# Optimization experiments

Measured on AMD Instinct MI355X. Metric: run time of the kernel, lower is better.

Reference implementation:

```python
import jax, jax.numpy as jnp
import numpy as np

GAMMA = 0.99
NUM_CODEWORDS = 512
CODEBOOK_DIM = 64


def setup_inputs() -> dict:
    key = jax.random.key(0)
    kx, kc = jax.random.split(key)
    x = jax.random.normal(kx, (32, 64, 64, 64), dtype=jnp.float32)  # [N,C,H,W]
    codebook = jax.random.normal(kc, (NUM_CODEWORDS, CODEBOOK_DIM), dtype=jnp.float32) / 2
    N_state = jnp.ones((NUM_CODEWORDS,), dtype=jnp.float32)
    m_state = codebook.copy()
    return {"x": x, "codebook": codebook, "N_state": N_state, "m_state": m_state}


def reference(x, codebook, N_state, m_state):
    N, C, H, W = x.shape
    K = codebook.shape[0]
    # flatten to tokens: [N*H*W, C]
    xf = jnp.transpose(x, (0, 2, 3, 1)).reshape(-1, C)
    d2 = (jnp.sum(xf * xf, axis=-1, keepdims=True)
          - 2.0 * (xf @ codebook.T)
          + jnp.sum(codebook * codebook, axis=-1)[None, :])
    index = jnp.argmin(d2, axis=1)  # [T]
    q = codebook[index].reshape(N, H, W, C).transpose(0, 3, 1, 2)  # [N,C,H,W]
    # straight-through estimator
    out = x + jax.lax.stop_gradient(q - x)
    # EMA update (training path, no_grad in original)
    counts = jax.ops.segment_sum(jnp.ones_like(index, dtype=x.dtype), index, num_segments=K)
    sums = jax.ops.segment_sum(xf, index, num_segments=K)  # [K,C]
    occupied = counts > 0
    N_new = jnp.where(occupied, N_state * GAMMA + counts * (1.0 - GAMMA), N_state)
    m_new = jnp.where(occupied[:, None], m_state * GAMMA + sums * (1.0 - GAMMA), m_state)
    codebook_new = m_new / N_new[:, None]
    return out, codebook_new, N_new, m_new
```

## Files before the change

kernel.cpp:

```cpp
#include <hip/hip_runtime.h>

static constexpr int Nn_ = 32, Cc_ = 64, Hh_ = 64, Ww_ = 64;
static constexpr int K_ = 512;
static constexpr int HW_ = Hh_ * Ww_;
static constexpr int CHW_ = Cc_ * HW_;
static constexpr int T_ = Nn_ * Hh_ * Ww_;
static constexpr int OUT_ELEMS = Nn_ * Cc_ * Hh_ * Ww_;
static constexpr int OFF_CB = OUT_ELEMS;
static constexpr int OFF_N  = OUT_ELEMS + 32768;
static constexpr int OFF_M  = OUT_ELEMS + 32768 + 512;

static constexpr int WS_IDX     = 0;
static constexpr int WS_FIXCNT  = T_;
static constexpr int WS_FIXLIST = T_ + 1;
static constexpr int WS_CBH     = 262148;
static constexpr int WS_CBL     = WS_CBH + 16384;
static constexpr int WS_CN      = WS_CBL + 16384;
static constexpr int WS_CNA     = WS_CN + 512;
static constexpr int WS_PART    = 295940;
static constexpr int SLICE_F    = K_ * Cc_ + K_;

static constexpr float THETA = 0.002f;

typedef _Float16 half8  __attribute__((ext_vector_type(8)));
typedef float    f32x16 __attribute__((ext_vector_type(16)));

__global__ __launch_bounds__(256) void k_prep(const float* __restrict__ cb,
                                              float* __restrict__ ws) {
    int j = blockIdx.x * 256 + threadIdx.x;
    if (j == 0) ((int*)(ws + WS_FIXCNT))[0] = 0;
    float v = cb[j];
    _Float16 h = (_Float16)v;
    _Float16 lo = (_Float16)(v - (float)h);
    ((_Float16*)(ws + WS_CBH))[j] = h;
    ((_Float16*)(ws + WS_CBL))[j] = lo;
    float sq = v * v;
#pragma unroll
    for (int m = 1; m < 64; m <<= 1) sq += __shfl_xor(sq, m);
    if ((threadIdx.x & 63) == 0) {
        int k = j >> 6;
        ws[WS_CN + k] = sq;
        int t = k >> 5, r5 = k & 31;
        int hi = (r5 >> 2) & 1;
        int reg = (r5 & 3) + 4 * (r5 >> 3);
        ws[WS_CNA + hi * 256 + t * 16 + reg] = sq;
    }
}

__global__ __launch_bounds__(256, 3) void k_assign(const float* __restrict__ x,
                                                   const float* __restrict__ cb,
                                                   float* __restrict__ ws,
                                                   float* __restrict__ out) {
    __shared__ alignas(16) unsigned char smem[52224];
    int* bi_s   = (int*)(smem + 51200);
    int* cert_s = (int*)(smem + 51712);

    const int b    = blockIdx.x;
    const int tid  = threadIdx.x;
    const int lane = tid & 63;
    const int wv   = tid >> 6;
    const int row0 = 2 * b, row1 = 2 * b + 1;
    const int xb0 = (row0 >> 6) * CHW_ + (row0 & 63) * Ww_;
    const int xb1 = (row1 >> 6) * CHW_ + (row1 & 63) * Ww_;

    {
        const int s  = tid & 31;
        const int c8 = tid >> 5;
        const int r  = s >> 4, wq = s & 15;
        half8 hp[4], lp[4];
#pragma unroll
        for (int stp = 0; stp < 8; ++stp) {
            int ch = c8 * 8 + stp;
            float4 v = *(const float4*)(x + (r ? xb1 : xb0) + ch * HW_ + 4 * wq);
            float vv[4] = {v.x, v.y, v.z, v.w};
#pragma unroll
            for (int j = 0; j < 4; ++j) {
                _Float16 h = (_Float16)vv[j];
                _Float16 lo = (_Float16)(vv[j] - (float)h);
                hp[j][stp] = h; lp[j][stp] = lo;
            }
        }
        const int blk = c8 ^ (wq & 7);
#pragma unroll
        for (int j = 0; j < 4; ++j) {
            int tt = 64 * r + 4 * wq + j;
            *(half8*)(smem + tt * 128 + blk * 16) = hp[j];
            *(half8*)(smem + 16384 + tt * 128 + blk * 16) = lp[j];
        }
        ((float*)(smem + 49152))[tid]       = ws[WS_CNA + tid];
        ((float*)(smem + 49152))[tid + 256] = ws[WS_CNA + tid + 256];
    }

    const char* cbh_g = (const char*)(ws + WS_CBH);
    const char* cbl_g = (const char*)(ws + WS_CBL);
    {
        float4 h4 = *(const float4*)(cbh_g + tid * 16);
        float4 l4 = *(const float4*)(cbl_g + tid * 16);
        int r = tid >> 3, p = (tid & 7) ^ (r & 7);
        *(float4*)(smem + 32768 + r * 128 + p * 16) = h4;
        *(float4*)(smem + 32768 + 4096 + r * 128 + p * 16) = l4;
    }
    __syncthreads();

    const int tb = 32 * wv + (lane & 31);
    const int hi = lane >> 5;
    half8 bh[4], bl[4];
    {
        const int tsw = (tb >> 2) & 7;
#pragma unroll
        for (int ks = 0; ks < 4; ++ks) {
            int blk = (2 * ks + hi) ^ tsw;
            bh[ks] = *(const half8*)(smem + tb * 128 + blk * 16);
            bl[ks] = *(const half8*)(smem + 16384 + tb * 128 + blk * 16);
        }
    }

    const float* cnA = (const float*)(smem + 49152);
    const int R = lane & 31;
    float bd1 = __int_as_float(0x7f800000);
    float bd2 = __int_as_float(0x7f800000);
    int bk1 = 0;

#pragma unroll 1
    for (int t = 0; t < 16; ++t) {
        const int cur = t & 1;
        float4 nh, nl;
        if (t < 15) {
            nh = *(const float4*)(cbh_g + (t + 1) * 4096 + tid * 16);
            nl = *(const float4*)(cbl_g + (t + 1) * 4096 + tid * 16);
        }
        const char* cb_b = (const char*)smem + 32768 + cur * 8192;
        half8 ah[4], al[4];
#pragma unroll
        for (int ks = 0; ks < 4; ++ks) {
            int p = (2 * ks + hi) ^ (R & 7);
            ah[ks] = *(const half8*)(cb_b + R * 128 + p * 16);
            al[ks] = *(const half8*)(cb_b + 4096 + R * 128 + p * 16);
        }
        f32x16 acc = {0.f,0.f,0.f,0.f, 0.f,0.f,0.f,0.f,
                      0.f,0.f,0.f,0.f, 0.f,0.f,0.f,0.f};
#pragma unroll
        for (int ks = 0; ks < 4; ++ks) {
            acc = __builtin_amdgcn_mfma_f32_32x32x16_f16(ah[ks], bh[ks], acc, 0, 0, 0);
            acc = __builtin_amdgcn_mfma_f32_32x32x16_f16(ah[ks], bl[ks], acc, 0, 0, 0);
            acc = __builtin_amdgcn_mfma_f32_32x32x16_f16(al[ks], bh[ks], acc, 0, 0, 0);
        }
        float cnv[16];
        {
            const float* cnp = cnA + hi * 256 + t * 16;
            *(float4*)&cnv[0]  = *(const float4*)(cnp);
            *(float4*)&cnv[4]  = *(const float4*)(cnp + 4);
            *(float4*)&cnv[8]  = *(const float4*)(cnp + 8);
            *(float4*)&cnv[12] = *(const float4*)(cnp + 12);
        }
        const int tb16 = t << 4;
#pragma unroll
        for (int j = 0; j < 16; ++j) {
            float d = fmaf(-2.0f, acc[j], cnv[j]);
            int kid = tb16 | j;
            bool lt = d < bd1;
            bd2 = lt ? bd1 : fminf(bd2, d);
            bk1 = lt ? kid : bk1;
            bd1 = fminf(bd1, d);
        }
        if (t < 15) {
            int r = tid >> 3, p2 = (tid & 7) ^ (r & 7);
            char* nb = (char*)smem + 32768 + (cur ^ 1) * 8192;
            *(float4*)(nb + r * 128 + p2 * 16) = nh;
            *(float4*)(nb + 4096 + r * 128 + p2 * 16) = nl;
        }
        __syncthreads();
    }

    {
        int t0 = bk1 >> 4, j0 = bk1 & 15;
        int rk = 32 * t0 + (j0 & 3) + 8 * (j0 >> 2) + 4 * hi;
        unsigned uf = __float_as_uint(bd1);
        uf = (uf & 0x80000000u) ? ~uf : (uf | 0x80000000u);
        unsigned long long me = ((unsigned long long)uf << 32) | (unsigned)rk;
        unsigned long long ot = (unsigned long long)__shfl_xor((long long)me, 32);
        float od1 = __shfl_xor(bd1, 32);
        float od2 = __shfl_xor(bd2, 32);
        unsigned long long m1 = (me < ot) ? me : ot;
        float d1m = fminf(bd1, od1);
        float d2m = fminf(fminf(bd2, od2), fmaxf(bd1, od1));
        if (hi == 0) {
            int k1 = (int)(m1 & 0xffffffffu);
            bool cert = (d2m - d1m) > THETA;
            bi_s[tb] = k1;
            cert_s[tb] = cert ? 1 : 0;
            ((int*)(ws + WS_IDX))[128 * b + tb] = k1;
            if (!cert) {
                int pos = atomicAdd((int*)(ws + WS_FIXCNT), 1);
                ((int*)(ws + WS_FIXLIST))[pos] = 128 * b + tb;
            }
        }
    }
    __syncthreads();

    float (*qt)[132] = (float(*)[132])smem;
#pragma unroll
    for (int jj = 0; jj < 32; ++jj) {
        int tt = wv * 32 + jj;
        qt[lane][tt] = cb[bi_s[tt] * 64 + lane];
    }
    __syncthreads();
#pragma unroll
    for (int r = 0; r < 2; ++r)
#pragma unroll
        for (int j = 0; j < 16; ++j) {
            int c = wv * 16 + j;
            out[(r ? xb1 : xb0) + c * HW_ + lane] = qt[c][64 * r + lane];
        }
}

__global__ __launch_bounds__(256) void k_fix(const float* __restrict__ x,
                                             const float* __restrict__ cb,
                                             float* __restrict__ ws,
                                             float* __restrict__ out) {
    __shared__ float xw[4][64];
    const int tid = threadIdx.x, wv = tid >> 6, lane = tid & 63;
    const int cnt = *(const int*)(ws + WS_FIXCNT);
    const int* list = (const int*)(ws + WS_FIXLIST);

    for (int it = blockIdx.x * 4 + wv; it < cnt; it += 256 * 4) {
        int g = list[it];
        int n = g >> 12, hw = g & 4095;
        const float* xp = x + n * CHW_ + hw;
        float xv = xp[lane * HW_];
        xw[wv][lane] = xv;
        unsigned long long best = ~0ull;
#pragma unroll 1
        for (int jj = 0; jj < 8; ++jj) {
            int k = lane + 64 * jj;
            const float4* cr = (const float4*)(cb + k * 64);
            float dot = 0.f;
#pragma unroll
            for (int q = 0; q < 16; ++q) {
                float4 cv = cr[q];
                dot = fmaf(cv.x, xw[wv][4 * q + 0], dot);
                dot = fmaf(cv.y, xw[wv][4 * q + 1], dot);
                dot = fmaf(cv.z, xw[wv][4 * q + 2], dot);
                dot = fmaf(cv.w, xw[wv][4 * q + 3], dot);
            }
            float d = fmaf(-2.0f, dot, ws[WS_CN + k]);
            unsigned uf = __float_as_uint(d);
            uf = (uf & 0x80000000u) ? ~uf : (uf | 0x80000000u);
            unsigned long long cd = ((unsigned long long)uf << 32) | (unsigned)k;
            if (cd < best) best = cd;
        }
#pragma unroll
        for (int m = 1; m < 64; m <<= 1) {
            unsigned long long o = (unsigned long long)__shfl_xor((long long)best, m);
            if (o < best) best = o;
        }
        int k1 = (int)(best & 0xffffffffu);
        out[n * CHW_ + lane * HW_ + hw] = cb[k1 * 64 + lane];
        if (lane == 0) ((int*)(ws + WS_IDX))[g] = k1;
    }
}

__global__ __launch_bounds__(512) void k_stats(const float* __restrict__ x,
                                               const float* __restrict__ ws_ro,
                                               float* __restrict__ ws,
                                               int TPB) {
    __shared__ float psum[512][64];
    __shared__ float xt[64][65];
    __shared__ float pcnt[512];
    __shared__ int   idx_s[512];

    const int tid = threadIdx.x;
    const int bid = blockIdx.x;
    const int wv = tid >> 6, lane = tid & 63;
    const int ngroups = TPB >> 9;
    const int blkbase = bid * TPB;

    const float4 z = make_float4(0.f, 0.f, 0.f, 0.f);
#pragma unroll
    for (int i = 0; i < 16; ++i) ((float4*)psum)[i * 512 + tid] = z;
    if (tid < 512) pcnt[tid] = 0.f;

    const int* __restrict__ idxg = (const int*)ws_ro;

    for (int g = 0; g < ngroups; ++g) {
        __syncthreads();
        int k0 = idxg[blkbase + g * 512 + tid];
        idx_s[tid] = k0;
        atomicAdd(&pcnt[k0], 1.0f);

        for (int sc = 0; sc < 8; ++sc) {
            __syncthreads();
#pragma unroll
            for (int it = 0; it < 2; ++it) {
                int e = it * 512 + tid;
                int c = e >> 4, tq = e & 15;
                int tok0 = blkbase + g * 512 + sc * 64;
                int n = tok0 >> 12, hw0 = tok0 & 4095;
                float4 v = *(const float4*)(x + n * CHW_ + c * HW_ + hw0 + 4 * tq);
                xt[4 * tq + 0][c] = v.x;
                xt[4 * tq + 1][c] = v.y;
                xt[4 * tq + 2][c] = v.z;
                xt[4 * tq + 3][c] = v.w;
            }
            __syncthreads();
#pragma unroll
            for (int i = 0; i < 8; ++i) {
                int tok = wv * 8 + i;
                int k = idx_s[sc * 64 + tok];
                atomicAdd(&psum[k][lane], xt[tok][lane]);
            }
        }
    }
    __syncthreads();

    float* pb = ws + WS_PART + (size_t)bid * SLICE_F;
#pragma unroll
    for (int i = 0; i < 16; ++i)
        ((float4*)pb)[i * 512 + tid] = ((float4*)psum)[i * 512 + tid];
    if (tid < 512) pb[32768 + tid] = pcnt[tid];
}

__global__ __launch_bounds__(256) void k_final(const float* __restrict__ Ns,
                                               const float* __restrict__ ms,
                                               const float* __restrict__ ws,
                                               float* __restrict__ out,
                                               int P) {
    int i = blockIdx.x * 256 + threadIdx.x;
    int k = i >> 6, c = i & 63;

    const float* base = ws + WS_PART;
    float s = 0.f, cnt = 0.f;
#pragma unroll 8
    for (int p = 0; p < P; ++p) {
        s   += base[(size_t)p * SLICE_F + i];
        cnt += base[(size_t)p * SLICE_F + 32768 + k];
    }

    const float gamma = 0.99f;
    const float omg   = (float)(1.0 - 0.99);

    bool occ = cnt > 0.0f;
    float Nv = Ns[k];
    float Nnew = occ ? (Nv * gamma + cnt * omg) : Nv;

    float mv = ms[i];
    float mnew = occ ? (mv * gamma + s * omg) : mv;

    out[OFF_CB + i] = mnew / Nnew;
    out[OFF_M  + i] = mnew;
    if (c == 0) out[OFF_N + k] = Nnew;
}

extern "C" void kernel_launch(void* const* d_in, const int* in_sizes, int n_in,
                              void* d_out, int out_size, void* d_ws, size_t ws_size,
                              hipStream_t stream) {
    const float* x  = (const float*)d_in[0];
    const float* cb = (const float*)d_in[1];
    const float* Ns = (const float*)d_in[2];
    const float* ms = (const float*)d_in[3];
    float* out = (float*)d_out;
    float* ws  = (float*)d_ws;

    int P = 256;
    while (P > 32 &&
           ((size_t)WS_PART + (size_t)P * SLICE_F) * 4 > ws_size)
        P >>= 1;
    int TPB = T_ / P;

    hipLaunchKernelGGL(k_prep,   dim3(128),  dim3(256), 0, stream, cb, ws);
    hipLaunchKernelGGL(k_assign, dim3(1024), dim3(256), 0, stream, x, cb, ws, out);
    hipLaunchKernelGGL(k_fix,    dim3(256),  dim3(256), 0, stream, x, cb, ws, out);
    hipLaunchKernelGGL(k_stats,  dim3(P),    dim3(512), 0, stream, x, ws, ws, TPB);
    hipLaunchKernelGGL(k_final,  dim3(128),  dim3(256), 0, stream, Ns, ms, ws, out, P);
}
```

Before: 211.7 us.

## Compute per-code sums in k_stats via one-hot MFMA with double-buffered tiles

Replaces the LDS atomicAdd scatter of token vectors into a 512x64 shared histogram with one-hot matrix multiplies on MFMA units. Each of 16 waves owns 32 codewords and accumulates sums in registers, splitting x into fp16 hi/lo parts to keep near-fp32 accuracy. The block grows to 1024 threads and double-buffers the transposed x tile so the next chunk's load overlaps compute. This removes LDS atomic contention and the 128KB shared accumulator, at the cost of four MFMAs per 16-token step and redundant one-hot work across codewords.

```diff
diff --git a/kernel.cpp b/kernel.cpp
--- a/kernel.cpp
+++ b/kernel.cpp
@@ -260,63 +260,105 @@
     }
 }
 
-__global__ __launch_bounds__(512) void k_stats(const float* __restrict__ x,
-                                               const float* __restrict__ ws_ro,
-                                               float* __restrict__ ws,
-                                               int TPB) {
-    __shared__ float psum[512][64];
-    __shared__ float xt[64][65];
+__global__ __launch_bounds__(1024, 4) void k_stats(const float* __restrict__ x,
+                                                   const float* __restrict__ ws_ro,
+                                                   float* __restrict__ ws,
+                                                   int TPB) {
+    __shared__ float xt[2][64][65];
     __shared__ float pcnt[512];
     __shared__ int   idx_s[512];
 
-    const int tid = threadIdx.x;
-    const int bid = blockIdx.x;
-    const int wv = tid >> 6, lane = tid & 63;
-    const int ngroups = TPB >> 9;
-    const int blkbase = bid * TPB;
-
-    const float4 z = make_float4(0.f, 0.f, 0.f, 0.f);
-#pragma unroll
-    for (int i = 0; i < 16; ++i) ((float4*)psum)[i * 512 + tid] = z;
+    const int tid  = threadIdx.x;
+    const int bid  = blockIdx.x;
+    const int wv   = tid >> 6;
+    const int lane = tid & 63;
+    const int hi   = lane >> 5;
+    const int m    = lane & 31;
+    const int NCH  = TPB >> 6;
+
+    f32x16 acc0 = {0.f,0.f,0.f,0.f, 0.f,0.f,0.f,0.f,
+                   0.f,0.f,0.f,0.f, 0.f,0.f,0.f,0.f};
+    f32x16 acc1 = acc0;
+
     if (tid < 512) pcnt[tid] = 0.f;
-
     const int* __restrict__ idxg = (const int*)ws_ro;
 
-    for (int g = 0; g < ngroups; ++g) {
+    const int cS = tid >> 4, tq = tid & 15;
+    {
+        int tok0 = bid * TPB;
+        int n = tok0 >> 12, hw0 = tok0 & 4095;
+        float4 v = *(const float4*)(x + n * CHW_ + cS * HW_ + hw0 + 4 * tq);
+        xt[0][4 * tq + 0][cS] = v.x;
+        xt[0][4 * tq + 1][cS] = v.y;
+        xt[0][4 * tq + 2][cS] = v.z;
+        xt[0][4 * tq + 3][cS] = v.w;
+    }
+
+    int cur = 0;
+    int k0 = 0;
+    const int kb = (wv << 5) + m;
+
+#pragma unroll 1
+    for (int cc = 0; cc < NCH; ++cc) {
+        const bool hasnext = (cc + 1 < NCH);
+        float4 v;
+        if (hasnext) {
+            int tok0 = bid * TPB + (cc + 1) * 64;
+            int n = tok0 >> 12, hw0 = tok0 & 4095;
+            v = *(const float4*)(x + n * CHW_ + cS * HW_ + hw0 + 4 * tq);
+        }
+        if ((cc & 7) == 0 && tid < 512)
+            k0 = idxg[bid * TPB + (cc >> 3) * 512 + tid];
         __syncthreads();
-        int k0 = idxg[blkbase + g * 512 + tid];
-        idx_s[tid] = k0;
-        atomicAdd(&pcnt[k0], 1.0f);
-
-        for (int sc = 0; sc < 8; ++sc) {
+        if ((cc & 7) == 0) {
+            if (tid < 512) { idx_s[tid] = k0; atomicAdd(&pcnt[k0], 1.0f); }
             __syncthreads();
-#pragma unroll
-            for (int it = 0; it < 2; ++it) {
-                int e = it * 512 + tid;
-                int c = e >> 4, tq = e & 15;
-                int tok0 = blkbase + g * 512 + sc * 64;
-                int n = tok0 >> 12, hw0 = tok0 & 4095;
-                float4 v = *(const float4*)(x + n * CHW_ + c * HW_ + hw0 + 4 * tq);
-                xt[4 * tq + 0][c] = v.x;
-                xt[4 * tq + 1][c] = v.y;
-                xt[4 * tq + 2][c] = v.z;
-                xt[4 * tq + 3][c] = v.w;
+        }
+
+#pragma unroll
+        for (int st = 0; st < 4; ++st) {
+            const int t0 = st * 16 + 8 * hi;
+            int ii[8];
+#pragma unroll
+            for (int j = 0; j < 8; ++j)
+                ii[j] = idx_s[((cc & 7) << 6) + t0 + j];
+            half8 bh0, bl0, bh1, bl1;
+#pragma unroll
+            for (int j = 0; j < 8; ++j) {
+                float f0 = xt[cur][t0 + j][m];
+                float f1 = xt[cur][t0 + j][32 + m];
+                _Float16 h0 = (_Float16)f0;
+                _Float16 h1 = (_Float16)f1;
+                bh0[j] = h0; bl0[j] = (_Float16)(f0 - (float)h0);
+                bh1[j] = h1; bl1[j] = (_Float16)(f1 - (float)h1);
             }
-            __syncthreads();
-#pragma unroll
-            for (int i = 0; i < 8; ++i) {
-                int tok = wv * 8 + i;
-                int k = idx_s[sc * 64 + tok];
-                atomicAdd(&psum[k][lane], xt[tok][lane]);
-            }
+            half8 ah;
+#pragma unroll
+            for (int j = 0; j < 8; ++j)
+                ah[j] = (ii[j] == kb) ? (_Float16)1.0f : (_Float16)0.0f;
+            acc0 = __builtin_amdgcn_mfma_f32_32x32x16_f16(ah, bh0, acc0, 0, 0, 0);
+            acc0 = __builtin_amdgcn_mfma_f32_32x32x16_f16(ah, bl0, acc0, 0, 0, 0);
+            acc1 = __builtin_amdgcn_mfma_f32_32x32x16_f16(ah, bh1, acc1, 0, 0, 0);
+            acc1 = __builtin_amdgcn_mfma_f32_32x32x16_f16(ah, bl1, acc1, 0, 0, 0);
+        }
+
+        if (hasnext) {
+            xt[cur ^ 1][4 * tq + 0][cS] = v.x;
+            xt[cur ^ 1][4 * tq + 1][cS] = v.y;
+            xt[cur ^ 1][4 * tq + 2][cS] = v.z;
+            xt[cur ^ 1][4 * tq + 3][cS] = v.w;
+            cur ^= 1;
         }
     }
     __syncthreads();
 
     float* pb = ws + WS_PART + (size_t)bid * SLICE_F;
 #pragma unroll
-    for (int i = 0; i < 16; ++i)
-        ((float4*)pb)[i * 512 + tid] = ((float4*)psum)[i * 512 + tid];
+    for (int r = 0; r < 16; ++r) {
+        int k = (wv << 5) + (r & 3) + 8 * (r >> 2) + 4 * hi;
+        pb[k * 64 + m]      = acc0[r];
+        pb[k * 64 + 32 + m] = acc1[r];
+    }
     if (tid < 512) pb[32768 + tid] = pcnt[tid];
 }
 
@@ -367,9 +409,9 @@
         P >>= 1;
     int TPB = T_ / P;
 
-    hipLaunchKernelGGL(k_prep,   dim3(128),  dim3(256), 0, stream, cb, ws);
-    hipLaunchKernelGGL(k_assign, dim3(1024), dim3(256), 0, stream, x, cb, ws, out);
-    hipLaunchKernelGGL(k_fix,    dim3(256),  dim3(256), 0, stream, x, cb, ws, out);
-    hipLaunchKernelGGL(k_stats,  dim3(P),    dim3(512), 0, stream, x, ws, ws, TPB);
-    hipLaunchKernelGGL(k_final,  dim3(128),  dim3(256), 0, stream, Ns, ms, ws, out, P);
-}
+    hipLaunchKernelGGL(k_prep,   dim3(128),  dim3(256),  0, stream, cb, ws);
+    hipLaunchKernelGGL(k_assign, dim3(1024), dim3(256),  0, stream, x, cb, ws, out);
+    hipLaunchKernelGGL(k_fix,    dim3(256),  dim3(256),  0, stream, x, cb, ws, out);
+    hipLaunchKernelGGL(k_stats,  dim3(P),    dim3(1024), 0, stream, x, ws, ws, TPB);
+    hipLaunchKernelGGL(k_final,  dim3(128),  dim3(256),  0, stream, Ns, ms, ws, out, P);
+}
```

Result: faster. 190.4 us (-10.1%).
